# Kernel tuning notes

Hardware: AMD Instinct MI355X
Metric: run time of the kernel (lower is better)

## Reference

```python
import jax, jax.numpy as jnp
from jax import lax
import numpy as np

B, H, W, C, N = 4, 512, 512, 32, 300000
K, S, P, D = 3, 2, 1, 1  # kernel, stride, padding, dilation


def setup_inputs() -> dict:
    key = jax.random.key(0)
    kf, _ = jax.random.split(key)
    features = jax.random.normal(kf, (N, C), dtype=jnp.float32)
    # unique active coordinates (spconv requires unique sites)
    rng = np.random.default_rng(0)
    lin = rng.choice(B * H * W, size=N, replace=False)
    b = lin // (H * W)
    y = (lin // W) % H
    x = lin % W
    coors = jnp.asarray(np.stack([b, y, x], axis=1), dtype=jnp.int32)  # [N,3]
    return {"features": features, "coors": coors, "batch_size": B}


def reference(features, coors, batch_size):
    # Scatter active features onto a dense grid initialized to -inf so that
    # inputs only; outputs with no active input in window are inactive).
    neg_inf = jnp.array(-jnp.inf, dtype=features.dtype)
    dense = jnp.full((batch_size, H, W, features.shape[1]), neg_inf,
                     dtype=features.dtype)
    b, y, x = coors[:, 0], coors[:, 1], coors[:, 2]
    dense = dense.at[b, y, x].set(features)  # coords are unique
    out = lax.reduce_window(
        dense, neg_inf, lax.max,
        window_dimensions=(1, K, K, 1),
        window_strides=(1, S, S, 1),
        padding=((0, 0), (P, P), (P, P), (0, 0)),
        window_dilation=(1, D, D, 1))
    # inactive output sites -> 0 (dense view of the sparse output tensor)
    return jnp.where(jnp.isinf(out), jnp.zeros((), out.dtype), out)
```

## Files before the change

kernel.cpp:

```cpp
#include <hip/hip_runtime.h>
#include <math.h>

#define BB 4
#define HH 512
#define WW 512
#define CC 32
#define HO 256
#define WO 256

__global__ void fill_zero_kernel(int4* __restrict__ g, int n4) {
    int i = blockIdx.x * blockDim.x + threadIdx.x;
    if (i < n4) g[i] = make_int4(0, 0, 0, 0);
}

__global__ void scatter_idx_kernel(const int* __restrict__ coors,
                                   int* __restrict__ grid, int n) {
    int i = blockIdx.x * blockDim.x + threadIdx.x;
    if (i >= n) return;
    int b = coors[i * 3 + 0];
    int y = coors[i * 3 + 1];
    int x = coors[i * 3 + 2];
    grid[((size_t)b * HH + y) * WW + x] = i + 1;
}

__global__ void __launch_bounds__(256)
pool_kernel(const float4* __restrict__ feat,
            const int* __restrict__ grid,
            float4* __restrict__ out) {
    int ox_base = (blockIdx.x & 7) * 32;
    int t       = (blockIdx.x >> 3) & 127;
    int b       = blockIdx.x >> 10;

    int tid = threadIdx.x;
    int cg  = tid & 7;
    int p   = tid >> 3;

    int iy0 = 4 * t - 1;
    int gx0 = 2 * ox_base - 1;
    const int* gb = grid + (size_t)b * (HH * WW);

    __shared__ int sg[5 * 66];

    for (int e = tid; e < 5 * 65; e += 256) {
        int r = e / 65;
        int c = e - r * 65;
        int iy = iy0 + r;
        int gx = gx0 + c;
        int v = 0;
        if ((unsigned)iy < (unsigned)HH && (unsigned)gx < (unsigned)WW)
            v = gb[iy * WW + gx];
        sg[r * 66 + c] = v;
    }
    __syncthreads();

    int lc = 2 * p;

    int v[15];
#pragma unroll
    for (int r = 0; r < 5; ++r)
#pragma unroll
        for (int dx = 0; dx < 3; ++dx)
            v[r * 3 + dx] = sg[r * 66 + lc + dx];

    float4 f[15];
#pragma unroll
    for (int k = 0; k < 15; ++k) {
        int r = v[k] - 1;
        r = r < 0 ? 0 : r;
        f[k] = feat[(size_t)r * 8 + cg];
    }

    const float NEG = -INFINITY;
    float4 acc0 = make_float4(NEG, NEG, NEG, NEG);
    float4 acc1 = make_float4(NEG, NEG, NEG, NEG);
#pragma unroll
    for (int k = 0; k < 15; ++k) {
        bool ok = v[k] != 0;
        float fx = ok ? f[k].x : NEG;
        float fy = ok ? f[k].y : NEG;
        float fz = ok ? f[k].z : NEG;
        float fw = ok ? f[k].w : NEG;
        if (k < 9) {
            acc0.x = fmaxf(acc0.x, fx);
            acc0.y = fmaxf(acc0.y, fy);
            acc0.z = fmaxf(acc0.z, fz);
            acc0.w = fmaxf(acc0.w, fw);
        }
        if (k >= 6) {
            acc1.x = fmaxf(acc1.x, fx);
            acc1.y = fmaxf(acc1.y, fy);
            acc1.z = fmaxf(acc1.z, fz);
            acc1.w = fmaxf(acc1.w, fw);
        }
    }

    acc0.x = isinf(acc0.x) ? 0.0f : acc0.x;
    acc0.y = isinf(acc0.y) ? 0.0f : acc0.y;
    acc0.z = isinf(acc0.z) ? 0.0f : acc0.z;
    acc0.w = isinf(acc0.w) ? 0.0f : acc0.w;
    acc1.x = isinf(acc1.x) ? 0.0f : acc1.x;
    acc1.y = isinf(acc1.y) ? 0.0f : acc1.y;
    acc1.z = isinf(acc1.z) ? 0.0f : acc1.z;
    acc1.w = isinf(acc1.w) ? 0.0f : acc1.w;

    int oy0  = 2 * t;
    size_t pos0 = ((size_t)(b * HO + oy0) * WO + ox_base + p);
    out[pos0 * 8 + cg]            = acc0;
    out[(pos0 + WO) * 8 + cg]     = acc1;
}

extern "C" void kernel_launch(void* const* d_in, const int* in_sizes, int n_in,
                              void* d_out, int out_size, void* d_ws, size_t ws_size,
                              hipStream_t stream) {
    const float* features = (const float*)d_in[0];
    const int*   coors    = (const int*)d_in[1];
    int n = in_sizes[0] / CC;

    int* grid = (int*)d_ws;

    {
        int n4 = (BB * HH * WW) / 4;
        int blk = 256, grd = (n4 + blk - 1) / blk;
        fill_zero_kernel<<<grd, blk, 0, stream>>>((int4*)grid, n4);
    }
    {
        int blk = 256, grd = (n + blk - 1) / blk;
        scatter_idx_kernel<<<grd, blk, 0, stream>>>(coors, grid, n);
    }
    {
        int grd = BB * (HO / 2) * (WO / 32);
        pool_kernel<<<grd, 256, 0, stream>>>((const float4*)features, grid,
                                             (float4*)d_out);
    }
}
```

Before: 110.0 us.

## Stage occupied tile features in shared memory to deduplicate gathers

The pool kernel now compacts the active sites in each 5x65 input halo tile into a shared list using an atomic counter. Each active feature row is then loaded once into shared memory with a rotated layout to avoid bank conflicts. Threads read their 15 window features from shared memory instead of issuing redundant global gathers, which cuts repeated global loads at overlapping windows. The cost is about 24KB of shared memory per block, which lowers occupancy, plus an extra sync, a shared atomic, and a global fallback path when a tile holds more than 192 active sites.

```diff
diff --git a/kernel.cpp b/kernel.cpp
--- a/kernel.cpp
+++ b/kernel.cpp
@@ -7,6 +7,8 @@
 #define CC 32
 #define HO 256
 #define WO 256
+
+#define MAXOCC 192
 
 __global__ void fill_zero_kernel(int4* __restrict__ g, int n4) {
     int i = blockIdx.x * blockDim.x + threadIdx.x;
@@ -39,7 +41,13 @@
     int gx0 = 2 * ox_base - 1;
     const int* gb = grid + (size_t)b * (HH * WW);
 
-    __shared__ int sg[5 * 66];
+    __shared__ int    smap[5 * 65];
+    __shared__ int    srcidx[MAXOCC];
+    __shared__ int    cnt;
+    __shared__ float4 sfeat[MAXOCC * 8];
+
+    if (tid == 0) cnt = 0;
+    __syncthreads();
 
     for (int e = tid; e < 5 * 65; e += 256) {
         int r = e / 65;
@@ -49,25 +57,39 @@
         int v = 0;
         if ((unsigned)iy < (unsigned)HH && (unsigned)gx < (unsigned)WW)
             v = gb[iy * WW + gx];
-        sg[r * 66 + c] = v;
+        int m = 0;
+        if (v != 0) {
+            int s = atomicAdd(&cnt, 1);
+            if (s < MAXOCC) { srcidx[s] = v - 1; m = s + 1; }
+            else            { m = -v; }
+        }
+        smap[e] = m;
+    }
+    __syncthreads();
+
+    int total = cnt < MAXOCC ? cnt : MAXOCC;
+    for (int s = (tid >> 3); s < total; s += 32) {
+        sfeat[(s << 3) + ((cg + s) & 7)] = feat[(size_t)srcidx[s] * 8 + cg];
     }
     __syncthreads();
 
     int lc = 2 * p;
-
-    int v[15];
+    int mm[15];
 #pragma unroll
     for (int r = 0; r < 5; ++r)
 #pragma unroll
         for (int dx = 0; dx < 3; ++dx)
-            v[r * 3 + dx] = sg[r * 66 + lc + dx];
+            mm[r * 3 + dx] = smap[r * 65 + lc + dx];
 
     float4 f[15];
 #pragma unroll
     for (int k = 0; k < 15; ++k) {
-        int r = v[k] - 1;
-        r = r < 0 ? 0 : r;
-        f[k] = feat[(size_t)r * 8 + cg];
+        int s = mm[k] > 0 ? mm[k] - 1 : 0;
+        f[k] = sfeat[(s << 3) + ((cg + s) & 7)];
+    }
+#pragma unroll
+    for (int k = 0; k < 15; ++k) {
+        if (mm[k] < 0) f[k] = feat[(size_t)(-mm[k] - 1) * 8 + cg];
     }
 
     const float NEG = -INFINITY;
@@ -75,7 +97,7 @@
     float4 acc1 = make_float4(NEG, NEG, NEG, NEG);
 #pragma unroll
     for (int k = 0; k < 15; ++k) {
-        bool ok = v[k] != 0;
+        bool ok = mm[k] != 0;
         float fx = ok ? f[k].x : NEG;
         float fy = ok ? f[k].y : NEG;
         float fz = ok ? f[k].z : NEG;
@@ -105,8 +127,8 @@
 
     int oy0  = 2 * t;
     size_t pos0 = ((size_t)(b * HO + oy0) * WO + ox_base + p);
-    out[pos0 * 8 + cg]            = acc0;
-    out[(pos0 + WO) * 8 + cg]     = acc1;
+    out[pos0 * 8 + cg]        = acc0;
+    out[(pos0 + WO) * 8 + cg] = acc1;
 }
 
 extern "C" void kernel_launch(void* const* d_in, const int* in_sizes, int n_in,
```

Result: faster. 107.5 us (-2.3%).
